# Performance work log

Hardware: AMD Instinct MI355X
Metric: run time of the kernel (lower is better)

## Reference

```python
import jax, jax.numpy as jnp
import numpy as np

N_NODES = 100000
N_EDGES = 1600000
IN_F = 67
H1, C1 = 10, 8   # heads, per-head channels layer 1
H2, C2 = 1, 1    # layer 2


def setup_inputs() -> dict:
    key = jax.random.key(0)
    ks = jax.random.split(key, 10)
    x = jax.random.normal(ks[0], (N_NODES, IN_F), dtype=jnp.float32)
    edge_index = jax.random.randint(ks[1], (2, N_EDGES), 0, N_NODES, dtype=jnp.int64)
    s = 0.1
    W1 = jax.random.normal(ks[2], (IN_F, H1 * C1), dtype=jnp.float32) * s
    att_src1 = jax.random.normal(ks[3], (H1, C1), dtype=jnp.float32) * s
    att_dst1 = jax.random.normal(ks[4], (H1, C1), dtype=jnp.float32) * s
    b1 = jnp.zeros((H1 * C1,), dtype=jnp.float32)
    W2 = jax.random.normal(ks[5], (H1 * C1, H2 * C2), dtype=jnp.float32) * s
    att_src2 = jax.random.normal(ks[6], (H2, C2), dtype=jnp.float32) * s
    att_dst2 = jax.random.normal(ks[7], (H2, C2), dtype=jnp.float32) * s
    b2 = jnp.zeros((H2 * C2,), dtype=jnp.float32)
    return {"x": x, "edge_index": edge_index, "W1": W1, "att_src1": att_src1,
            "att_dst1": att_dst1, "b1": b1, "W2": W2, "att_src2": att_src2,
            "att_dst2": att_dst2, "b2": b2}


def gat_conv(x, src, dst, W, att_src, att_dst, bias, heads, out_ch):
    """PyG GATConv (eval mode): gather -> leaky_relu -> segment softmax -> scatter."""
    n = x.shape[0]
    h = (x @ W).reshape(n, heads, out_ch)                     # [N,H,C]
    a_src = jnp.sum(h * att_src, axis=-1)                     # [N,H]
    a_dst = jnp.sum(h * att_dst, axis=-1)                     # [N,H]
    e = a_src[src] + a_dst[dst]                               # [E,H]
    e = jax.nn.leaky_relu(e, negative_slope=0.2)
    # numerically stable softmax over edges grouped by destination node
    m = jax.ops.segment_max(e, dst, num_segments=n)           # [N,H]
    ex = jnp.exp(e - m[dst])
    denom = jax.ops.segment_sum(ex, dst, num_segments=n)      # [N,H]
    alpha = ex / denom[dst]                                   # [E,H]
    msg = h[src] * alpha[:, :, None]                          # [E,H,C]
    out = jax.ops.segment_sum(msg, dst, num_segments=n)       # [N,H,C]
    return out.reshape(n, heads * out_ch) + bias


def reference(x, edge_index, W1, att_src1, att_dst1, b1, W2, att_src2, att_dst2, b2):
    n = x.shape[0]
    loops = jnp.arange(n, dtype=edge_index.dtype)
    src = jnp.concatenate([edge_index[0], loops])             # add_self_loops=True
    dst = jnp.concatenate([edge_index[1], loops])
    h = gat_conv(x, src, dst, W1, att_src1, att_dst1, b1, H1, C1)
    h = jax.nn.elu(h)
    out = gat_conv(h, src, dst, W2, att_src2, att_dst2, b2, H2, C2)
    return out
```

## Files before the change

kernel.cpp:

```cpp
#include <hip/hip_runtime.h>
#include <math.h>

#define IN_F 67
#define F1   80
#define NH1  10
#define NC1  8

#define GN   64
#define KS   104
#define PKS  96

#define CB    512
#define CSH   9
#define NBC   196
#define RB    64
#define NGRP  8
#define GCAP  1536
#define SLCAP 1664
#define CSTRIDE 16
#define NFB   512
#define CHUNK 2048

typedef _Float16 h16;
typedef h16 h16x2 __attribute__((ext_vector_type(2)));
typedef h16 h16x8 __attribute__((ext_vector_type(8)));
typedef float f32x4 __attribute__((ext_vector_type(4)));
typedef float f32x4u __attribute__((ext_vector_type(4), aligned(4)));
typedef int i32x4 __attribute__((ext_vector_type(4)));

__global__ __launch_bounds__(256)
void k_front(const float* __restrict__ x, const float* __restrict__ W,
             const float* __restrict__ att_s, const float* __restrict__ att_d,
             const int* __restrict__ ei, int* __restrict__ gcur,
             int* __restrict__ ebuf, h16* __restrict__ pk,
             float* __restrict__ a_dst, int N, int E) {
    __shared__ __align__(16) char smem[GN * 81 * 4];
    const int tid = threadIdx.x;

    if ((int)blockIdx.x < NFB) {
        int2* sStage = (int2*)smem;
        int*  sCnt   = (int*)(smem + CHUNK * 8);
        int*  sGBase = sCnt + NBC;
        int*  sScan  = sGBase + NBC;
        const int g = blockIdx.x & (NGRP - 1);

        for (int base_e = blockIdx.x * CHUNK; base_e < E; base_e += NFB * CHUNK) {
            int lim = E - base_e; if (lim > CHUNK) lim = CHUNK;
            for (int i = tid; i < NBC; i += 256) sCnt[i] = 0;
            __syncthreads();

            int2 ev[8]; int pos[8]; int nloc = 0;
            int e0 = base_e + tid * 8;
            if (tid * 8 + 8 <= lim) {
                i32x4 s0 = *(const i32x4*)(ei + e0);
                i32x4 s1 = *(const i32x4*)(ei + e0 + 4);
                i32x4 d0 = *(const i32x4*)(ei + E + e0);
                i32x4 d1 = *(const i32x4*)(ei + E + e0 + 4);
#pragma unroll
                for (int j = 0; j < 4; ++j) { ev[j] = make_int2(s0[j], d0[j]); }
#pragma unroll
                for (int j = 0; j < 4; ++j) { ev[4 + j] = make_int2(s1[j], d1[j]); }
                nloc = 8;
            } else {
                for (int j = 0; j < 8; ++j) {
                    int e = e0 + j;
                    if (tid * 8 + j < lim) { ev[nloc++] = make_int2(ei[e], ei[E + e]); }
                }
            }
            for (int j = 0; j < nloc; ++j)
                pos[j] = atomicAdd(&sCnt[ev[j].y >> CSH], 1);
            __syncthreads();

            int v = (tid < NBC) ? sCnt[tid] : 0;
            sScan[tid] = v;
            __syncthreads();
            for (int o = 1; o < 256; o <<= 1) {
                int u = (tid >= o) ? sScan[tid - o] : 0;
                __syncthreads();
                sScan[tid] += u;
                __syncthreads();
            }
            for (int j = 0; j < nloc; ++j) {
                int B = ev[j].y >> CSH;
                sStage[sScan[B] - sCnt[B] + pos[j]] = ev[j];
            }
            if (tid < NBC && sCnt[tid] > 0)
                sGBase[tid] = atomicAdd(&gcur[((size_t)g * NBC + tid) * CSTRIDE], sCnt[tid]);
            __syncthreads();

            int total = sScan[NBC - 1];
            for (int i = tid; i < total; i += 256) {
                int2 e = sStage[i];
                int B = e.y >> CSH;
                int gp = sGBase[B] + (i - (sScan[B] - sCnt[B]));
                if (gp < GCAP)
                    ebuf[((size_t)g * NBC + B) * GCAP + gp] = e.x | ((e.y & (CB - 1)) << 17);
            }
            __syncthreads();
        }
        return;
    }

    h16*   sWt = (h16*)smem;
    float* sO  = (float*)smem;
    const int node0 = (blockIdx.x - NFB) * GN;

    if (tid < 240) {
        int c = tid - (tid >= 160 ? 160 : (tid >= 80 ? 80 : 0));
        int kb = (tid >= 160 ? 64 : (tid >= 80 ? 32 : 0));
        h16 tmp[32];
#pragma unroll
        for (int j = 0; j < 32; ++j) {
            int k = kb + j;
            tmp[j] = (h16)((k < IN_F) ? W[k * F1 + c] : 0.f);
        }
        h16* dst = sWt + c * KS + kb;
#pragma unroll
        for (int j = 0; j < 4; ++j)
            *(h16x8*)(dst + j * 8) = *(const h16x8*)(tmp + j * 8);
    }
    __syncthreads();

    const int lane = tid & 63;
    const int m    = lane & 15;
    const int quad = lane >> 4;
    const int wn0  = (tid >> 6) * 16;

    int gn  = node0 + wn0 + m;
    int gnc = gn < N ? gn : N - 1;
    const float* xr = x + (size_t)gnc * IN_F;

    f32x4 acc[5];
#pragma unroll
    for (int ct = 0; ct < 5; ++ct) acc[ct] = (f32x4){0.f, 0.f, 0.f, 0.f};

#pragma unroll
    for (int ks = 0; ks < 64; ks += 32) {
        int k0 = ks + quad * 8;
        f32x4 a0 = *(const f32x4u*)(xr + k0);
        f32x4 a1 = *(const f32x4u*)(xr + k0 + 4);
        h16x8 af;
        af[0] = (h16)a0.x; af[1] = (h16)a0.y; af[2] = (h16)a0.z; af[3] = (h16)a0.w;
        af[4] = (h16)a1.x; af[5] = (h16)a1.y; af[6] = (h16)a1.z; af[7] = (h16)a1.w;
#pragma unroll
        for (int ct = 0; ct < 5; ++ct) {
            h16x8 bf = *(const h16x8*)(sWt + (ct * 16 + m) * KS + ks + quad * 8);
            acc[ct] = __builtin_amdgcn_mfma_f32_16x16x32_f16(af, bf, acc[ct], 0, 0, 0);
        }
    }
    {
        h16x8 af = (h16x8)(h16)0.f;
        if (quad == 0) {
            af[0] = (h16)xr[64]; af[1] = (h16)xr[65]; af[2] = (h16)xr[66];
        }
#pragma unroll
        for (int ct = 0; ct < 5; ++ct) {
            h16x8 bf = *(const h16x8*)(sWt + (ct * 16 + m) * KS + 64 + quad * 8);
            acc[ct] = __builtin_amdgcn_mfma_f32_16x16x32_f16(af, bf, acc[ct], 0, 0, 0);
        }
    }
    __syncthreads();

#pragma unroll
    for (int ct = 0; ct < 5; ++ct)
#pragma unroll
        for (int r = 0; r < 4; ++r)
            sO[(wn0 + quad * 4 + r) * 81 + ct * 16 + m] = acc[ct][r];
    __syncthreads();

    for (int idx = tid; idx < GN * (F1 / 2); idx += 256) {
        int n = idx / (F1 / 2);
        int p = idx - n * (F1 / 2);
        int gg = node0 + n;
        if (gg < N) {
            h16x2 v;
            v.x = (h16)sO[n * 81 + 2 * p];
            v.y = (h16)sO[n * 81 + 2 * p + 1];
            *(h16x2*)(pk + (size_t)gg * PKS + 2 * p) = v;
        }
    }
    for (int t = tid; t < GN * NH1; t += 256) {
        int n = t / NH1;
        int h = t - n * NH1;
        int gg = node0 + n;
        if (gg < N) {
            const float* hr = sO + n * 81 + h * NC1;
            float s = 0.f, d = 0.f;
#pragma unroll
            for (int c = 0; c < NC1; ++c) {
                float v = hr[c];
                s += v * att_s[h * NC1 + c];
                d += v * att_d[h * NC1 + c];
            }
            pk[(size_t)gg * PKS + F1 + h] = (h16)s;
            a_dst[gg * NH1 + h] = d;
        }
    }
}

__global__ __launch_bounds__(256)
void k_agg1(const int* __restrict__ ebuf, const int* __restrict__ gcur,
            const h16* __restrict__ pk, const float* __restrict__ a_dst,
            const float* __restrict__ b1, const float* __restrict__ W2,
            const float* __restrict__ att_s2, const float* __restrict__ att_d2,
            float2* __restrict__ hs2, float* __restrict__ a_dst2,
            int* __restrict__ row, int* __restrict__ deg, int* __restrict__ csr2,
            int N, int NB) {
    __shared__ int   sTmp[SLCAP];
    __shared__ int   sList[SLCAP];
    __shared__ int   s_cnt[RB];
    __shared__ int   s_scan[RB];
    __shared__ int   s_cur[RB];
    __shared__ float s_acc[RB];
    __shared__ int   sTot;

    const int tid = threadIdx.x;
    const int b = blockIdx.x;
    const int B = b >> 3;
    const int q = b & 7;
    const int lo = b * RB;

    for (int i = tid; i < RB; i += 256) { s_cnt[i] = 1; s_acc[i] = 0.f; }
    if (tid == 0) sTot = 0;
    __syncthreads();

    for (int g = 0; g < NGRP; ++g) {
        size_t slot = (size_t)g * NBC + B;
        int cnt = gcur[slot * CSTRIDE];
        cnt = cnt < GCAP ? cnt : GCAP;
        const int* eb = ebuf + slot * GCAP;
        for (int i = tid; i < cnt; i += 256) {
            int v = eb[i];
            int dloc = v >> 17;
            if ((dloc >> 6) == q) {
                int n_l = dloc & (RB - 1);
                atomicAdd(&s_cnt[n_l], 1);
                int p = atomicAdd(&sTot, 1);
                if (p < SLCAP) sTmp[p] = (v & 0x1FFFF) | (n_l << 17);
            }
        }
    }
    __syncthreads();

    if (tid < RB) s_scan[tid] = s_cnt[tid];
    __syncthreads();
    for (int o = 1; o < RB; o <<= 1) {
        int v = 0;
        if (tid < RB && tid >= o) v = s_scan[tid - o];
        __syncthreads();
        if (tid < RB) s_scan[tid] += v;
        __syncthreads();
    }
    if (tid < RB) {
        int excl = s_scan[tid] - s_cnt[tid];
        int n = lo + tid;
        if (excl < SLCAP) sList[excl] = n;
        s_cur[tid] = excl + 1;
        if (n < N) {
            int dg = s_cnt[tid];
            if (excl + dg > SLCAP) dg = SLCAP - excl > 0 ? SLCAP - excl : 0;
            row[n] = b * SLCAP + excl;
            deg[n] = dg;
        }
    }
    __syncthreads();

    int total = sTot < SLCAP ? sTot : SLCAP;
    for (int i = tid; i < total; i += 256) {
        int u = sTmp[i];
        int n_l = u >> 17;
        int p = atomicAdd(&s_cur[n_l], 1);
        if (p < SLCAP) sList[p] = u & 0x1FFFF;
    }
    __syncthreads();

    int tot2 = s_scan[RB - 1];
    tot2 = tot2 < SLCAP ? tot2 : SLCAP;
    for (int i = tid; i < tot2; i += 256)
        csr2[(size_t)b * SLCAP + i] = sList[i];

    for (int t = tid; t < RB * NH1; t += 256) {
        int n_l = t / NH1;
        int h = t - n_l * NH1;
        int n = lo + n_l;
        if (n >= N) continue;
        int beg = s_scan[n_l] - s_cnt[n_l];
        int end = beg + s_cnt[n_l];
        end = end < SLCAP ? end : SLCAP;
        float ad = a_dst[n * NH1 + h];
        float den = 0.f;
        float num[NC1];
#pragma unroll
        for (int c = 0; c < NC1; ++c) num[c] = 0.f;

        int i = beg;
        for (; i + 3 < end; i += 4) {
            int sv[4];
#pragma unroll
            for (int j = 0; j < 4; ++j) sv[j] = sList[i + j];
            h16x8 qf[4];
            float a[4];
#pragma unroll
            for (int j = 0; j < 4; ++j) {
                const h16* rp = pk + (size_t)sv[j] * PKS;
                qf[j] = *(const h16x8*)(rp + h * NC1);
                a[j] = (float)rp[F1 + h];
            }
#pragma unroll
            for (int j = 0; j < 4; ++j) {
                float v = a[j] + ad;
                v = v > 0.f ? v : 0.2f * v;
                float w = __expf(v);
                den += w;
#pragma unroll
                for (int c = 0; c < NC1; ++c) num[c] += w * (float)qf[j][c];
            }
        }
        for (; i < end; ++i) {
            const h16* rp = pk + (size_t)sList[i] * PKS;
            h16x8 qf = *(const h16x8*)(rp + h * NC1);
            float v = (float)rp[F1 + h] + ad;
            v = v > 0.f ? v : 0.2f * v;
            float w = __expf(v);
            den += w;
#pragma unroll
            for (int c = 0; c < NC1; ++c) num[c] += w * (float)qf[c];
        }
        float inv = 1.f / den;
        const float* bb = b1 + h * NC1;
        const float* w2 = W2 + h * NC1;
        float p = 0.f;
#pragma unroll
        for (int c = 0; c < NC1; ++c) {
            float o = num[c] * inv + bb[c];
            o = o > 0.f ? o : expm1f(o);
            p += o * w2[c];
        }
        atomicAdd(&s_acc[n_l], p);
    }
    __syncthreads();

    if (tid < RB) {
        int n = lo + tid;
        if (n < N) {
            float acc = s_acc[tid];
            float2 v;
            v.x = acc;
            v.y = acc * att_s2[0];
            hs2[n] = v;
            a_dst2[n] = acc * att_d2[0];
        }
    }
}

__global__ __launch_bounds__(256)
void k_agg2(const int* __restrict__ row, const int* __restrict__ deg,
            const int* __restrict__ csr2, const float2* __restrict__ hs2,
            const float* __restrict__ a_dst2, const float* __restrict__ b2,
            float* __restrict__ out, int N) {
    int n = blockIdx.x * blockDim.x + threadIdx.x;
    if (n >= N) return;
    float ad = a_dst2[n];
    float den = 0.f, num = 0.f;
    int beg = row[n];
    int end = beg + deg[n];
    int i = beg;
    for (; i + 7 < end; i += 8) {
        int sv[8];
#pragma unroll
        for (int j = 0; j < 8; ++j) sv[j] = csr2[i + j];
        float2 g[8];
#pragma unroll
        for (int j = 0; j < 8; ++j) g[j] = hs2[sv[j]];
#pragma unroll
        for (int j = 0; j < 8; ++j) {
            float v = g[j].y + ad;
            v = v > 0.f ? v : 0.2f * v;
            float w = __expf(v);
            den += w;
            num += w * g[j].x;
        }
    }
    for (; i < end; ++i) {
        float2 g = hs2[csr2[i]];
        float v = g.y + ad;
        v = v > 0.f ? v : 0.2f * v;
        float w = __expf(v);
        den += w;
        num += w * g.x;
    }
    out[n] = num / den + b2[0];
}

extern "C" void kernel_launch(void* const* d_in, const int* in_sizes, int n_in,
                              void* d_out, int out_size, void* d_ws, size_t ws_size,
                              hipStream_t stream) {
    const float* x        = (const float*)d_in[0];
    const int*   ei       = (const int*)d_in[1];
    const float* W1       = (const float*)d_in[2];
    const float* att_src1 = (const float*)d_in[3];
    const float* att_dst1 = (const float*)d_in[4];
    const float* b1       = (const float*)d_in[5];
    const float* W2       = (const float*)d_in[6];
    const float* att_src2 = (const float*)d_in[7];
    const float* att_dst2 = (const float*)d_in[8];
    const float* b2       = (const float*)d_in[9];
    float* out = (float*)d_out;

    const int N  = in_sizes[0] / IN_F;
    const int E  = in_sizes[1] / 2;
    const int NB = (N + RB - 1) / RB;

    float*  ws      = (float*)d_ws;
    h16*    pk      = (h16*)ws;
    float*  a_dst1  = ws + (size_t)N * (PKS / 2);
    float2* hs2     = (float2*)(a_dst1 + (size_t)N * NH1);
    float*  a_dst2  = (float*)(hs2 + N);
    int*    row     = (int*)(a_dst2 + N);
    int*    deg     = row + N;
    int*    gcur    = deg + N;
    int*    csr2    = gcur + (size_t)NGRP * NBC * CSTRIDE;
    int*    ebuf    = csr2 + (size_t)NB * SLCAP;

    const int B = 256;
    const int nbG = (N + GN - 1) / GN;

    hipMemsetAsync(gcur, 0, (size_t)NGRP * NBC * CSTRIDE * sizeof(int), stream);
    k_front<<<NFB + nbG, 256, 0, stream>>>(x, W1, att_src1, att_dst1, ei,
                                           gcur, ebuf, pk, a_dst1, N, E);

    k_agg1<<<NB, 256, 0, stream>>>(ebuf, gcur, pk, a_dst1, b1, W2,
                                   att_src2, att_dst2, hs2, a_dst2,
                                   row, deg, csr2, N, NB);

    k_agg2<<<(N + B - 1) / B, B, 0, stream>>>(row, deg, csr2, hs2, a_dst2, b2, out, N);
}
```

Baseline: 216.3 us.

## Use wave-shuffle scans, ballot-aggregated atomics, and 4 lanes per node in agg2

The shared-memory Hillis-Steele scans in the front binning and agg1 kernels become wavefront shuffle scans, which removes many block-wide barriers. The agg1 edge-filtering loop now takes one slot per wave from the sTot atomic, chosen by ballot and popcount, instead of one atomic per matching edge. The global bucket atomicAdd is moved earlier so it overlaps with the staging scatter. k_agg2 now gives each node four lanes that split its edge list and combine partial sums by xor shuffle, which adds parallelism and memory-level concurrency at the cost of more threads and a shuffle reduction.

```diff
diff --git a/kernel.cpp b/kernel.cpp
--- a/kernel.cpp
+++ b/kernel.cpp
@@ -20,6 +20,7 @@
 #define CSTRIDE 16
 #define NFB   512
 #define CHUNK 2048
+#define A2T   4
 
 typedef _Float16 h16;
 typedef h16 h16x2 __attribute__((ext_vector_type(2)));
@@ -42,7 +43,10 @@
         int*  sCnt   = (int*)(smem + CHUNK * 8);
         int*  sGBase = sCnt + NBC;
         int*  sScan  = sGBase + NBC;
+        int*  wsum   = sScan + 256;
         const int g = blockIdx.x & (NGRP - 1);
+        const int lane = tid & 63;
+        const int wv = tid >> 6;
 
         for (int base_e = blockIdx.x * CHUNK; base_e < E; base_e += NFB * CHUNK) {
             int lim = E - base_e; if (lim > CHUNK) lim = CHUNK;
@@ -72,20 +76,26 @@
             __syncthreads();
 
             int v = (tid < NBC) ? sCnt[tid] : 0;
-            sScan[tid] = v;
-            __syncthreads();
-            for (int o = 1; o < 256; o <<= 1) {
-                int u = (tid >= o) ? sScan[tid - o] : 0;
-                __syncthreads();
-                sScan[tid] += u;
-                __syncthreads();
-            }
+            int sc = v;
+#pragma unroll
+            for (int o = 1; o < 64; o <<= 1) {
+                int u = __shfl_up(sc, o);
+                if (lane >= o) sc += u;
+            }
+            if (lane == 63) wsum[wv] = sc;
+            __syncthreads();
+            int add = 0;
+#pragma unroll
+            for (int w = 0; w < 4; ++w) add += (w < wv) ? wsum[w] : 0;
+            sScan[tid] = sc + add;
+            if (tid < NBC && v > 0)
+                sGBase[tid] = atomicAdd(&gcur[((size_t)g * NBC + tid) * CSTRIDE], v);
+            __syncthreads();
+
             for (int j = 0; j < nloc; ++j) {
                 int B = ev[j].y >> CSH;
                 sStage[sScan[B] - sCnt[B] + pos[j]] = ev[j];
             }
-            if (tid < NBC && sCnt[tid] > 0)
-                sGBase[tid] = atomicAdd(&gcur[((size_t)g * NBC + tid) * CSTRIDE], sCnt[tid]);
             __syncthreads();
 
             int total = sScan[NBC - 1];
@@ -215,6 +225,7 @@
     __shared__ int   sTot;
 
     const int tid = threadIdx.x;
+    const int lane = tid & 63;
     const int b = blockIdx.x;
     const int B = b >> 3;
     const int q = b & 7;
@@ -229,35 +240,44 @@
         int cnt = gcur[slot * CSTRIDE];
         cnt = cnt < GCAP ? cnt : GCAP;
         const int* eb = ebuf + slot * GCAP;
-        for (int i = tid; i < cnt; i += 256) {
-            int v = eb[i];
-            int dloc = v >> 17;
-            if ((dloc >> 6) == q) {
-                int n_l = dloc & (RB - 1);
+        for (int i0 = 0; i0 < cnt; i0 += 256) {
+            int i = i0 + tid;
+            int v = 0, n_l = 0;
+            bool match = false;
+            if (i < cnt) {
+                v = eb[i];
+                int dloc = v >> 17;
+                match = (dloc >> 6) == q;
+                n_l = dloc & (RB - 1);
+            }
+            unsigned long long mk = __ballot(match);
+            int base = 0;
+            if (lane == 0 && mk) base = atomicAdd(&sTot, __popcll(mk));
+            base = __shfl(base, 0);
+            if (match) {
                 atomicAdd(&s_cnt[n_l], 1);
-                int p = atomicAdd(&sTot, 1);
+                int p = base + __popcll(mk & ((1ull << lane) - 1));
                 if (p < SLCAP) sTmp[p] = (v & 0x1FFFF) | (n_l << 17);
             }
         }
     }
     __syncthreads();
 
-    if (tid < RB) s_scan[tid] = s_cnt[tid];
-    __syncthreads();
-    for (int o = 1; o < RB; o <<= 1) {
-        int v = 0;
-        if (tid < RB && tid >= o) v = s_scan[tid - o];
-        __syncthreads();
-        if (tid < RB) s_scan[tid] += v;
-        __syncthreads();
-    }
     if (tid < RB) {
-        int excl = s_scan[tid] - s_cnt[tid];
+        int cntv = s_cnt[tid];
+        int sc = cntv;
+#pragma unroll
+        for (int o = 1; o < RB; o <<= 1) {
+            int u = __shfl_up(sc, o);
+            if (tid >= o) sc += u;
+        }
+        s_scan[tid] = sc;
+        int excl = sc - cntv;
         int n = lo + tid;
         if (excl < SLCAP) sList[excl] = n;
         s_cur[tid] = excl + 1;
         if (n < N) {
-            int dg = s_cnt[tid];
+            int dg = cntv;
             if (excl + dg > SLCAP) dg = SLCAP - excl > 0 ? SLCAP - excl : 0;
             row[n] = b * SLCAP + excl;
             deg[n] = dg;
@@ -358,38 +378,37 @@
             const int* __restrict__ csr2, const float2* __restrict__ hs2,
             const float* __restrict__ a_dst2, const float* __restrict__ b2,
             float* __restrict__ out, int N) {
-    int n = blockIdx.x * blockDim.x + threadIdx.x;
+    int t = blockIdx.x * blockDim.x + threadIdx.x;
+    int n = t >> 2;
+    int sl = t & (A2T - 1);
     if (n >= N) return;
     float ad = a_dst2[n];
+    int beg = row[n];
+    int dg  = deg[n];
     float den = 0.f, num = 0.f;
-    int beg = row[n];
-    int end = beg + deg[n];
-    int i = beg;
-    for (; i + 7 < end; i += 8) {
-        int sv[8];
-#pragma unroll
-        for (int j = 0; j < 8; ++j) sv[j] = csr2[i + j];
-        float2 g[8];
-#pragma unroll
-        for (int j = 0; j < 8; ++j) g[j] = hs2[sv[j]];
-#pragma unroll
-        for (int j = 0; j < 8; ++j) {
-            float v = g[j].y + ad;
-            v = v > 0.f ? v : 0.2f * v;
-            float w = __expf(v);
-            den += w;
-            num += w * g[j].x;
-        }
-    }
-    for (; i < end; ++i) {
-        float2 g = hs2[csr2[i]];
+    int i = sl;
+    for (; i + A2T < dg; i += 2 * A2T) {
+        int s0 = csr2[beg + i];
+        int s1 = csr2[beg + i + A2T];
+        float2 g0 = hs2[s0];
+        float2 g1 = hs2[s1];
+        float v0 = g0.y + ad; v0 = v0 > 0.f ? v0 : 0.2f * v0;
+        float v1 = g1.y + ad; v1 = v1 > 0.f ? v1 : 0.2f * v1;
+        float w0 = __expf(v0), w1 = __expf(v1);
+        den += w0 + w1;
+        num += w0 * g0.x + w1 * g1.x;
+    }
+    for (; i < dg; i += A2T) {
+        float2 g = hs2[csr2[beg + i]];
         float v = g.y + ad;
         v = v > 0.f ? v : 0.2f * v;
         float w = __expf(v);
         den += w;
         num += w * g.x;
     }
-    out[n] = num / den + b2[0];
+    den += __shfl_xor(den, 1); num += __shfl_xor(num, 1);
+    den += __shfl_xor(den, 2); num += __shfl_xor(num, 2);
+    if (sl == 0) out[n] = num / den + b2[0];
 }
 
 extern "C" void kernel_launch(void* const* d_in, const int* in_sizes, int n_in,
@@ -433,5 +452,6 @@
                                    att_src2, att_dst2, hs2, a_dst2,
                                    row, deg, csr2, N, NB);
 
-    k_agg2<<<(N + B - 1) / B, B, 0, stream>>>(row, deg, csr2, hs2, a_dst2, b2, out, N);
+    k_agg2<<<((size_t)N * A2T + B - 1) / B, B, 0, stream>>>(row, deg, csr2, hs2,
+                                                            a_dst2, b2, out, N);
 }
```

Result: no change. 216.3 us (+0.0%).
